# Kernel optimization log

Hardware: AMD Instinct MI355X
Metric: run time of the kernel (lower is better)

Reference implementation:

```python
import jax, jax.numpy as jnp
import numpy as np

H = 32  # hidden size (hardcoded in source module)

def setup_inputs() -> dict:
    key = jax.random.key(0)
    ks = jax.random.split(key, 7)
    s = 1.0 / np.sqrt(H)  # PyTorch LSTM/Linear init scale
    return {
        "x":    jax.random.normal(ks[0], (8192, 512, 1), dtype=jnp.float32),
        "W_ih": jax.random.uniform(ks[1], (4 * H, 1), minval=-s, maxval=s, dtype=jnp.float32),
        "W_hh": jax.random.uniform(ks[2], (4 * H, H), minval=-s, maxval=s, dtype=jnp.float32),
        "b_ih": jax.random.uniform(ks[3], (4 * H,), minval=-s, maxval=s, dtype=jnp.float32),
        "b_hh": jax.random.uniform(ks[4], (4 * H,), minval=-s, maxval=s, dtype=jnp.float32),
        "W_fc": jax.random.uniform(ks[5], (1, H), minval=-s, maxval=s, dtype=jnp.float32),
        "b_fc": jax.random.uniform(ks[6], (1,), minval=-s, maxval=s, dtype=jnp.float32),
    }

def reference(x, W_ih, W_hh, b_ih, b_hh, W_fc, b_fc):
    B = x.shape[0]
    # Precompute input projections for all timesteps: [B, T, 4H]
    xg = jnp.einsum('bti,gi->btg', x, W_ih) + (b_ih + b_hh)
    xg_t = jnp.swapaxes(xg, 0, 1)  # [T, B, 4H] for scan over time

    def step(carry, xgt):
        h, c = carry
        gates = xgt + h @ W_hh.T           # [B, 4H]
        i, f, g, o = jnp.split(gates, 4, axis=-1)  # PyTorch gate order i,f,g,o
        i = jax.nn.sigmoid(i)
        f = jax.nn.sigmoid(f)
        g = jnp.tanh(g)
        o = jax.nn.sigmoid(o)
        c = f * c + i * g
        h = o * jnp.tanh(c)
        return (h, c), None

    h0 = jnp.zeros((B, H), dtype=x.dtype)
    c0 = jnp.zeros((B, H), dtype=x.dtype)
    (h_last, _), _ = jax.lax.scan(step, (h0, c0), xg_t)
    # Final linear head on last timestep hidden state: [B, output_size]
    return h_last @ W_fc.T + b_fc
```

## Files before the change

kernel.cpp:

```cpp
#include <hip/hip_runtime.h>


#define TT 512
#define HH 32
#define L2E 1.44269504088896340736f
#define XROW 132
#define HROW 40

typedef _Float16 f16x8 __attribute__((ext_vector_type(8)));
typedef float f32x4 __attribute__((ext_vector_type(4)));

__device__ __forceinline__ float fastrcp(float x) { return __builtin_amdgcn_rcpf(x); }
__device__ __forceinline__ float exp2f_(float x) { return __builtin_amdgcn_exp2f(x); }

__launch_bounds__(512, 4)
__global__ void lstm_kernel(const float* __restrict__ x,
                            const float* __restrict__ W_ih,
                            const float* __restrict__ W_hh,
                            const float* __restrict__ b_ih,
                            const float* __restrict__ b_hh,
                            const float* __restrict__ W_fc,
                            const float* __restrict__ b_fc,
                            float* __restrict__ out) {
    __shared__ _Float16 hh[2][16][HROW];
    __shared__ _Float16 hl[2][16][HROW];
    __shared__ float xbuf[16 * XROW];

    const int tid  = threadIdx.x;
    const int lane = tid & 63;
    const int w    = tid >> 6;
    const int c    = lane & 15;
    const int q    = lane >> 4;
    const int base = blockIdx.x * 16;

    const int gate = c & 3;
    const float asc = (gate == 2) ? (2.0f * L2E) : (-L2E);
    const int wrow0 = gate * 32 + 8 * (c >> 2);
    f16x8 wa;
    #pragma unroll
    for (int j = 0; j < 8; ++j)
        wa[j] = (_Float16)(W_hh[(wrow0 + w) * HH + 8 * q + j] * asc);

    const int u = 8 * q + w;
    f32x4 wih, bcs;
    #pragma unroll
    for (int r = 0; r < 4; ++r) {
        const float sc = (r == 2) ? (2.0f * L2E) : (-L2E);
        wih[r] = W_ih[32 * r + u] * sc;
        bcs[r] = (b_ih[32 * r + u] + b_hh[32 * r + u]) * sc;
    }

    for (int i = tid; i < 16 * HROW; i += 512) {
        ((_Float16*)hh[0])[i] = (_Float16)0.f;
        ((_Float16*)hl[0])[i] = (_Float16)0.f;
    }

    const int xr  = tid >> 5;
    const int xc4 = (tid & 31) * 4;
    {
        const float4 v = *(const float4*)&x[(size_t)(base + xr) * TT + xc4];
        *(float4*)&xbuf[xr * XROW + xc4] = v;
    }

    float cs = 0.f;
    float xc = 0.f;
    f32x4 ai;

    #pragma unroll 1
    for (int t = 0; t < TT; ++t) {
        const int RP = t & 1;
        if ((t & 127) == 0) {
            if (t) {
                const float4 v = *(const float4*)&x[(size_t)(base + xr) * TT + t + xc4];
                *(float4*)&xbuf[xr * XROW + xc4] = v;
            }
            __syncthreads();
            xc = xbuf[c * XROW];
            ai = wih * xc + bcs;
        }
        const f16x8 BH = *(const f16x8*)&hh[RP][c][8 * q];
        const f16x8 BL = *(const f16x8*)&hl[RP][c][8 * q];
        __builtin_amdgcn_s_setprio(1);
        f32x4 a = __builtin_amdgcn_mfma_f32_16x16x32_f16(wa, BH, ai, 0, 0, 0);
        a = __builtin_amdgcn_mfma_f32_16x16x32_f16(wa, BL, a, 0, 0, 0);
        const float xn = xbuf[c * XROW + ((t + 1) & 127)];
        const float Ei = exp2f_(a[0]);
        const float Ef = exp2f_(a[1]);
        const float G  = exp2f_(a[2]);
        const float Eo = exp2f_(a[3]);
        const float aig = (1.f + Ei) * (G + 1.f);
        const float af  = 1.f + Ef;
        const float num = cs * aig + (G - 1.f) * af;
        const float den = af * aig;
        const float cn  = num * fastrcp(den);
        cs = cn;
        const float ycv = __builtin_amdgcn_fmed3f(cn * (2.0f * L2E), -60.f, 60.f);
        const float C   = exp2f_(ycv);
        const float hden = (C + 1.f) * (1.f + Eo);
        const float hv   = (C - 1.f) * fastrcp(hden);
        __builtin_amdgcn_s_setprio(0);
        const _Float16 ph = (_Float16)hv;
        const _Float16 pl = (_Float16)(hv - (float)ph);
        hh[RP ^ 1][c][u] = ph;
        hl[RP ^ 1][c][u] = pl;
        ai = wih * xn + bcs;
        __syncthreads();
        xc = xn;
    }

    if (w == 0) {
        const f16x8 BH = *(const f16x8*)&hh[0][c][8 * q];
        const f16x8 BL = *(const f16x8*)&hl[0][c][8 * q];
        float s = 0.f;
        #pragma unroll
        for (int j = 0; j < 8; ++j)
            s += ((float)BH[j] + (float)BL[j]) * W_fc[8 * q + j];
        s += __shfl_xor(s, 16);
        s += __shfl_xor(s, 32);
        if (lane < 16)
            out[base + lane] = b_fc[0] + s;
    }
}

extern "C" void kernel_launch(void* const* d_in, const int* in_sizes, int n_in,
                              void* d_out, int out_size, void* d_ws, size_t ws_size,
                              hipStream_t stream) {
    const float* x    = (const float*)d_in[0];
    const float* W_ih = (const float*)d_in[1];
    const float* W_hh = (const float*)d_in[2];
    const float* b_ih = (const float*)d_in[3];
    const float* b_hh = (const float*)d_in[4];
    const float* W_fc = (const float*)d_in[5];
    const float* b_fc = (const float*)d_in[6];
    float* out = (float*)d_out;

    const int B = 8192;
    lstm_kernel<<<B / 16, 512, 0, stream>>>(x, W_ih, W_hh, b_ih, b_hh,
                                            W_fc, b_fc, out);
}
```

Before: 275.6 us.

## Repack h buffers into XOR-swizzled layout and split MFMA accumulation chains

Replaces the padded [16][40] hidden-state LDS arrays with a packed 512-element layout in which each lane's eight-element read is contiguous and the per-lane writes are XOR-swizzled by quarter. The W_hh register fragment is permuted to match. The goal is to cut LDS bank conflicts on the per-step scalar writes and vector reads. The two MFMAs now accumulate independently (the second starts from zero) and are summed afterward, which removes the dependency between them at the cost of an extra vector add. The final FC head is rewritten to read from the swizzled layout.

Result: no change. 280.3 us (+1.7%).

```diff
diff --git a/kernel.cpp b/kernel.cpp
--- a/kernel.cpp
+++ b/kernel.cpp
@@ -5,7 +5,6 @@
 #define HH 32
 #define L2E 1.44269504088896340736f
 #define XROW 132
-#define HROW 40
 
 typedef _Float16 f16x8 __attribute__((ext_vector_type(8)));
 typedef float f32x4 __attribute__((ext_vector_type(4)));
@@ -22,8 +21,8 @@
                             const float* __restrict__ W_fc,
                             const float* __restrict__ b_fc,
                             float* __restrict__ out) {
-    __shared__ _Float16 hh[2][16][HROW];
-    __shared__ _Float16 hl[2][16][HROW];
+    __shared__ _Float16 hhp[2][512];
+    __shared__ _Float16 hlp[2][512];
     __shared__ float xbuf[16 * XROW];
 
     const int tid  = threadIdx.x;
@@ -38,8 +37,10 @@
     const int wrow0 = gate * 32 + 8 * (c >> 2);
     f16x8 wa;
     #pragma unroll
-    for (int j = 0; j < 8; ++j)
-        wa[j] = (_Float16)(W_hh[(wrow0 + w) * HH + 8 * q + j] * asc);
+    for (int j = 0; j < 8; ++j) {
+        const int u = 8 * q + (j ^ (2 * q));
+        wa[j] = (_Float16)(W_hh[(wrow0 + w) * HH + u] * asc);
+    }
 
     const int u = 8 * q + w;
     f32x4 wih, bcs;
@@ -50,9 +51,12 @@
         bcs[r] = (b_ih[32 * r + u] + b_hh[32 * r + u]) * sc;
     }
 
-    for (int i = tid; i < 16 * HROW; i += 512) {
-        ((_Float16*)hh[0])[i] = (_Float16)0.f;
-        ((_Float16*)hl[0])[i] = (_Float16)0.f;
+    const int rdo = q * 128 + c * 8;
+    const int wro = rdo + (w ^ (2 * q));
+
+    for (int i = tid; i < 512; i += 512) {
+        hhp[0][i] = (_Float16)0.f;
+        hlp[0][i] = (_Float16)0.f;
     }
 
     const int xr  = tid >> 5;
@@ -63,7 +67,6 @@
     }
 
     float cs = 0.f;
-    float xc = 0.f;
     f32x4 ai;
 
     #pragma unroll 1
@@ -75,15 +78,17 @@
                 *(float4*)&xbuf[xr * XROW + xc4] = v;
             }
             __syncthreads();
-            xc = xbuf[c * XROW];
+            const float xc = xbuf[c * XROW];
             ai = wih * xc + bcs;
         }
-        const f16x8 BH = *(const f16x8*)&hh[RP][c][8 * q];
-        const f16x8 BL = *(const f16x8*)&hl[RP][c][8 * q];
+        const f16x8 BH = *(const f16x8*)&hhp[RP][rdo];
+        const f16x8 BL = *(const f16x8*)&hlp[RP][rdo];
         __builtin_amdgcn_s_setprio(1);
-        f32x4 a = __builtin_amdgcn_mfma_f32_16x16x32_f16(wa, BH, ai, 0, 0, 0);
-        a = __builtin_amdgcn_mfma_f32_16x16x32_f16(wa, BL, a, 0, 0, 0);
+        const f32x4 z = {0.f, 0.f, 0.f, 0.f};
+        const f32x4 a0 = __builtin_amdgcn_mfma_f32_16x16x32_f16(wa, BH, ai, 0, 0, 0);
+        const f32x4 a1 = __builtin_amdgcn_mfma_f32_16x16x32_f16(wa, BL, z, 0, 0, 0);
         const float xn = xbuf[c * XROW + ((t + 1) & 127)];
+        const f32x4 a = a0 + a1;
         const float Ei = exp2f_(a[0]);
         const float Ef = exp2f_(a[1]);
         const float G  = exp2f_(a[2]);
@@ -101,24 +106,21 @@
         __builtin_amdgcn_s_setprio(0);
         const _Float16 ph = (_Float16)hv;
         const _Float16 pl = (_Float16)(hv - (float)ph);
-        hh[RP ^ 1][c][u] = ph;
-        hl[RP ^ 1][c][u] = pl;
+        hhp[RP ^ 1][wro] = ph;
+        hlp[RP ^ 1][wro] = pl;
         ai = wih * xn + bcs;
         __syncthreads();
-        xc = xn;
     }
 
-    if (w == 0) {
-        const f16x8 BH = *(const f16x8*)&hh[0][c][8 * q];
-        const f16x8 BL = *(const f16x8*)&hl[0][c][8 * q];
-        float s = 0.f;
+    if (tid < 16) {
+        float s = b_fc[0];
         #pragma unroll
-        for (int j = 0; j < 8; ++j)
-            s += ((float)BH[j] + (float)BL[j]) * W_fc[8 * q + j];
-        s += __shfl_xor(s, 16);
-        s += __shfl_xor(s, 32);
-        if (lane < 16)
-            out[base + lane] = b_fc[0] + s;
+        for (int uu = 0; uu < 32; ++uu) {
+            const int qb = uu >> 3;
+            const int off = qb * 128 + tid * 8 + ((uu & 7) ^ (2 * qb));
+            s += ((float)hhp[0][off] + (float)hlp[0][off]) * W_fc[uu];
+        }
+        out[base + tid] = s;
     }
 }
 
```
